# Kernel tuning notes

Hardware: AMD Instinct MI355X
Metric: run time of the kernel (lower is better)

Reference implementation:

```python
import jax, jax.numpy as jnp
import numpy as np

B, S, D, H, FF = 4, 2048, 1024, 16, 4096
DT, TARGET, ITERS = 0.1, 0.0, 5


def _ln(x, w, b):
    mu = jnp.mean(x, axis=-1, keepdims=True)
    var = jnp.mean((x - mu) ** 2, axis=-1, keepdims=True)
    return (x - mu) * jax.lax.rsqrt(var + 1e-5) * w + b


def setup_inputs() -> dict:
    key = jax.random.key(0)
    ks = iter(jax.random.split(key, 16))
    w = lambda shape: jax.random.normal(next(ks), shape, dtype=jnp.float32) * 0.02
    return {
        "x": jax.random.normal(next(ks), (B, S, D), dtype=jnp.float32),
        "ln_attn_w": jnp.ones((D,), jnp.float32), "ln_attn_b": jnp.zeros((D,), jnp.float32),
        "attn_in_w": w((3 * D, D)), "attn_in_b": jnp.zeros((3 * D,), jnp.float32),
        "attn_out_w": w((D, D)), "attn_out_b": jnp.zeros((D,), jnp.float32),
        "ln1_w": jnp.ones((D,), jnp.float32), "ln1_b": jnp.zeros((D,), jnp.float32),
        "ln2_w": jnp.ones((D,), jnp.float32), "ln2_b": jnp.zeros((D,), jnp.float32),
        "inl_u_w": w((D, D)), "inl_u_b": jnp.zeros((D,), jnp.float32),
        "inl_a_w": w((D, D)), "inl_a_b": jnp.zeros((D,), jnp.float32),
        "inl_b_w": w((D, D)), "inl_b_b": jnp.zeros((D,), jnp.float32),
        "inl_g_w": w((D, D)), "inl_g_b": jnp.zeros((D,), jnp.float32),
        "ff1_w": w((FF, D)), "ff1_b": jnp.zeros((FF,), jnp.float32),
        "ff2_w": w((D, FF)), "ff2_b": jnp.zeros((D,), jnp.float32),
    }


def reference(x, ln_attn_w, ln_attn_b, attn_in_w, attn_in_b, attn_out_w, attn_out_b,
              ln1_w, ln1_b, ln2_w, ln2_b,
              inl_u_w, inl_u_b, inl_a_w, inl_a_b, inl_b_w, inl_b_b, inl_g_w, inl_g_b,
              ff1_w, ff1_b, ff2_w, ff2_b):
    dh = D // H
    scale = 1.0 / np.sqrt(dh).astype(np.float32)
    # --- causal multi-head attention (dropout = identity, eval mode) ---
    xn = _ln(x, ln_attn_w, ln_attn_b)
    qkv = xn @ attn_in_w.T + attn_in_b            # [B,S,3D]
    q, k, v = jnp.split(qkv, 3, axis=-1)
    hsplit = lambda t: t.reshape(B, S, H, dh).transpose(0, 2, 1, 3)  # [B,H,S,dh]
    q, k, v = hsplit(q), hsplit(k), hsplit(v)
    scores = jnp.einsum('bhqd,bhkd->bhqk', q, k) * scale
    causal = jnp.triu(jnp.ones((S, S), dtype=bool), 1)
    scores = jnp.where(causal, jnp.finfo(scores.dtype).min, scores)
    probs = jax.nn.softmax(scores, axis=-1)
    attn_out = jnp.einsum('bhqk,bhkd->bhqd', probs, v).transpose(0, 2, 1, 3).reshape(B, S, D)
    attn_out = attn_out @ attn_out_w.T + attn_out_b
    x = x + attn_out
    context = attn_out
    # --- INL integrator dynamics (controllers depend only on context) ---
    xs = _ln(x, ln1_w, ln1_b)
    vs = jnp.zeros_like(xs)
    u = context @ inl_u_w.T + inl_u_b
    alpha = jax.nn.sigmoid(context @ inl_a_w.T + inl_a_b)
    beta = jax.nn.softplus(context @ inl_b_w.T + inl_b_b)
    g = jax.nn.sigmoid(context @ inl_g_w.T + inl_g_b)
    for _ in range(ITERS):
        vs = vs + DT * (alpha * (TARGET - xs) - beta * vs + u)
        xs = xs + DT * g * vs
    x = x + xs
    # --- feed-forward (exact GELU as torch default) ---
    h = _ln(x, ln2_w, ln2_b)
    x = x + (jax.nn.gelu(h @ ff1_w.T + ff1_b, approximate=False) @ ff2_w.T + ff2_b)
    return x
```

## Files before the change

kernel.cpp:

```cpp
#include <hip/hip_runtime.h>
#include <cstdint>
#include <cmath>

typedef __attribute__((ext_vector_type(4))) float floatx4;
typedef __attribute__((ext_vector_type(8))) __bf16 bf16x8;
typedef __attribute__((ext_vector_type(4))) unsigned short ushort4v;

#define DEVI static __device__ __forceinline__

DEVI unsigned short f2b(float f) {
    unsigned x = __float_as_uint(f);
    return (unsigned short)((x + 0x7fffu + ((x >> 16) & 1u)) >> 16);
}
DEVI float b2f(unsigned short u) { return __uint_as_float(((unsigned)u) << 16); }

DEVI void load16(void* lds, const void* g) {
    __builtin_amdgcn_global_load_lds(
        (__attribute__((address_space(1))) void*)(const_cast<void*>(g)),
        (__attribute__((address_space(3))) void*)lds, 16, 0, 0);
}

DEVI floatx4 MFMA16(bf16x8 a, bf16x8 b, floatx4 c) {
    return __builtin_amdgcn_mfma_f32_16x16x32_bf16(a, b, c, 0, 0, 0);
}

__global__ __launch_bounds__(256) void cvt_kernel(const float* __restrict__ src,
                                                  unsigned short* __restrict__ dst, int n4) {
    int i = blockIdx.x * 256 + threadIdx.x;
    if (i >= n4) return;
    floatx4 v = ((const floatx4*)src)[i];
    ushort4v o;
    o[0] = f2b(v[0]); o[1] = f2b(v[1]); o[2] = f2b(v[2]); o[3] = f2b(v[3]);
    ((ushort4v*)dst)[i] = o;
}

__global__ __launch_bounds__(256) void catbias_kernel(const float* __restrict__ a,
                                                      const float* __restrict__ b,
                                                      const float* __restrict__ c,
                                                      const float* __restrict__ d,
                                                      float* __restrict__ o) {
    int i = blockIdx.x * 256 + threadIdx.x;
    int p = i >> 10, j = i & 1023;
    float v = (p == 0) ? a[j] : (p == 1) ? b[j] : (p == 2) ? c[j] : d[j];
    o[i] = v;
}

__global__ __launch_bounds__(256) void ln_kernel(const float* __restrict__ in,
                                                 const float* __restrict__ w,
                                                 const float* __restrict__ b,
                                                 unsigned short* __restrict__ obf,
                                                 float* __restrict__ of) {
    const int row = blockIdx.x, tid = threadIdx.x;
    const floatx4* pr = (const floatx4*)(in + (size_t)row * 1024);
    floatx4 v = pr[tid];
    float s  = v[0] + v[1] + v[2] + v[3];
    float ss = v[0]*v[0] + v[1]*v[1] + v[2]*v[2] + v[3]*v[3];
    #pragma unroll
    for (int o = 32; o >= 1; o >>= 1) { s += __shfl_xor(s, o); ss += __shfl_xor(ss, o); }
    __shared__ float red[8];
    int wv = tid >> 6, lane = tid & 63;
    if (lane == 0) { red[wv] = s; red[4 + wv] = ss; }
    __syncthreads();
    s  = red[0] + red[1] + red[2] + red[3];
    ss = red[4] + red[5] + red[6] + red[7];
    float mu  = s * (1.0f / 1024.0f);
    float var = ss * (1.0f / 1024.0f) - mu * mu;
    float rstd = rsqrtf(var + 1e-5f);
    floatx4 wv4 = ((const floatx4*)w)[tid];
    floatx4 bv4 = ((const floatx4*)b)[tid];
    floatx4 o;
    #pragma unroll
    for (int c = 0; c < 4; c++) o[c] = (v[c] - mu) * rstd * wv4[c] + bv4[c];
    if (obf) {
        ushort4v t;
        t[0] = f2b(o[0]); t[1] = f2b(o[1]); t[2] = f2b(o[2]); t[3] = f2b(o[3]);
        ((ushort4v*)(obf + (size_t)row * 1024))[tid] = t;
    }
    if (of) ((floatx4*)(of + (size_t)row * 1024))[tid] = o;
}

__global__ __launch_bounds__(256) void integrator_kernel(const float* __restrict__ xs0,
                                                         const unsigned short* __restrict__ uabg,
                                                         float* __restrict__ xio) {
    size_t i = (size_t)blockIdx.x * 256 + threadIdx.x;
    size_t tok = i >> 8;
    int grp = (int)(i & 255) * 4;
    const unsigned short* ubase = uabg + tok * 4096 + grp;
    ushort4v uu = *(const ushort4v*)(ubase);
    ushort4v aa = *(const ushort4v*)(ubase + 1024);
    ushort4v bb = *(const ushort4v*)(ubase + 2048);
    ushort4v gg = *(const ushort4v*)(ubase + 3072);
    floatx4 xsv = ((const floatx4*)xs0)[i];
    floatx4 x1  = ((const floatx4*)xio)[i];
    floatx4 res;
    #pragma unroll
    for (int c = 0; c < 4; c++) {
        float u = b2f(uu[c]), a = b2f(aa[c]), bt = b2f(bb[c]), g = b2f(gg[c]);
        float xs = xsv[c], vs = 0.f;
        #pragma unroll
        for (int t = 0; t < 5; t++) {
            vs += 0.1f * (-a * xs - bt * vs + u);
            xs += 0.1f * g * vs;
        }
        res[c] = x1[c] + xs;
    }
    ((floatx4*)xio)[i] = res;
}

template <int EPI, int KP>
__global__ __launch_bounds__(512, 2) void gemm8(const unsigned short* __restrict__ A,
                                                const unsigned short* __restrict__ W,
                                                const float* __restrict__ bias,
                                                unsigned short* __restrict__ ob0,
                                                unsigned short* __restrict__ ob1,
                                                unsigned short* __restrict__ ob2,
                                                float* __restrict__ of0,
                                                const float* __restrict__ xres) {
    constexpr int NT = KP / 64;
    __shared__ unsigned short sA[2][2][256 * 32];
    __shared__ unsigned short sB[2][2][256 * 32];
    const int tid = threadIdx.x;
    const int wave = tid >> 6, lane = tid & 63;
    const int ln = lane & 15, quad = lane >> 4;
    const int wr = wave >> 2, wc = wave & 3;

    const int gx = gridDim.x;
    const int flat = blockIdx.y * gx + blockIdx.x;
    const int cpx = (gx * (int)gridDim.y) >> 3;
    const int rmp = (flat & 7) * cpx + (flat >> 3);
    const size_t m0 = (size_t)(rmp / gx) * 256;
    const int n0 = (rmp % gx) * 256;

    floatx4 acc[8][4];
    #pragma unroll
    for (int mt = 0; mt < 8; mt++)
        #pragma unroll
        for (int nt = 0; nt < 4; nt++) acc[mt][nt] = floatx4{0.f, 0.f, 0.f, 0.f};

    const int srow = tid >> 2;
    const int sgr  = (tid & 3) ^ (srow & 3);
    const unsigned short* gAs = A + (m0 + srow) * KP + sgr * 8;
    const unsigned short* gBs = W + ((size_t)(n0 + srow)) * KP + sgr * 8;
    const size_t jstride = (size_t)128 * KP;
    const int sbase = wave * 512;

    const int csw  = (quad ^ (ln & 3)) * 8;
    const int arow = (wr * 128 + ln) * 32 + csw;
    const int brow = (wc * 64 + ln) * 32 + csw;

    auto stageA = [&](int buf, int kk, int t) {
        const unsigned short* s = gAs + (size_t)t * 64 + kk * 32;
        load16(&sA[buf][kk][sbase], s);
        load16(&sA[buf][kk][sbase + 4096], s + jstride);
    };
    auto stageB = [&](int buf, int kk, int t) {
        const unsigned short* s = gBs + (size_t)t * 64 + kk * 32;
        load16(&sB[buf][kk][sbase], s);
        load16(&sB[buf][kk][sbase + 4096], s + jstride);
    };

    bf16x8 af[8], bq0, bq1;
    auto ldA = [&](int buf, int kk) {
        #pragma unroll
        for (int mt = 0; mt < 8; mt++)
            af[mt] = *(const bf16x8*)&sA[buf][kk][arow + mt * 512];
    };
    auto ldB = [&](int buf, int kk, int nh) {
        bq0 = *(const bf16x8*)&sB[buf][kk][brow + nh * 1024];
        bq1 = *(const bf16x8*)&sB[buf][kk][brow + nh * 1024 + 512];
    };
    auto mma = [&](int nh) {
        __builtin_amdgcn_sched_barrier(0);
        __builtin_amdgcn_s_setprio(1);
        #pragma unroll
        for (int mt = 0; mt < 8; mt++) {
            acc[mt][nh * 2]     = MFMA16(af[mt], bq0, acc[mt][nh * 2]);
            acc[mt][nh * 2 + 1] = MFMA16(af[mt], bq1, acc[mt][nh * 2 + 1]);
        }
        __builtin_amdgcn_s_setprio(0);
        __builtin_amdgcn_sched_barrier(0);
    };

    stageA(0, 0, 0); stageB(0, 0, 0); stageA(0, 1, 0); stageB(0, 1, 0);
    asm volatile("s_waitcnt vmcnt(4)" ::: "memory");
    asm volatile("s_barrier" ::: "memory");

    auto tilestep = [&](int kt, int buf, bool last) {
        ldA(buf, 0); ldB(buf, 0, 0);
        if (!last) stageA(buf ^ 1, 0, kt + 1);
        asm volatile("s_barrier" ::: "memory");
        asm volatile("s_waitcnt lgkmcnt(0)" ::: "memory");
        mma(0);
        asm volatile("s_barrier" ::: "memory");
        ldB(buf, 0, 1);
        if (!last) {
            stageB(buf ^ 1, 0, kt + 1);
            asm volatile("s_waitcnt vmcnt(4)" ::: "memory");
        } else {
            asm volatile("s_waitcnt vmcnt(0)" ::: "memory");
        }
        asm volatile("s_barrier" ::: "memory");
        asm volatile("s_waitcnt lgkmcnt(0)" ::: "memory");
        mma(1);
        asm volatile("s_barrier" ::: "memory");
        ldA(buf, 1); ldB(buf, 1, 0);
        if (!last) stageA(buf ^ 1, 1, kt + 1);
        asm volatile("s_barrier" ::: "memory");
        asm volatile("s_waitcnt lgkmcnt(0)" ::: "memory");
        mma(0);
        asm volatile("s_barrier" ::: "memory");
        ldB(buf, 1, 1);
        if (!last) {
            stageB(buf ^ 1, 1, kt + 1);
            asm volatile("s_waitcnt vmcnt(4)" ::: "memory");
        }
        asm volatile("s_barrier" ::: "memory");
        asm volatile("s_waitcnt lgkmcnt(0)" ::: "memory");
        mma(1);
        asm volatile("s_barrier" ::: "memory");
    };

    #pragma unroll 1
    for (int kt = 0; kt < NT - 2; kt += 2) {
        tilestep(kt, 0, false);
        tilestep(kt + 1, 1, false);
    }
    tilestep(NT - 2, 0, false);
    tilestep(NT - 1, 1, true);

    const size_t rowb = m0 + wr * 128 + quad * 4;
    const int colb = n0 + wc * 64 + ln;
    #pragma unroll
    for (int mt = 0; mt < 8; mt++) {
        #pragma unroll
        for (int nt = 0; nt < 4; nt++) {
            const int n = colb + nt * 16;
            const float bs = bias[n];
            #pragma unroll
            for (int r = 0; r < 4; r++) {
                const size_t row = rowb + mt * 16 + r;
                float c = acc[mt][nt][r] + bs;
                if constexpr (EPI == 0) {
                    int sect = n >> 10, d1 = n & 1023, h = d1 >> 6, d = d1 & 63;
                    int bb = (int)(row >> 11), s = (int)(row & 2047);
                    size_t bh = (size_t)(bb * 16 + h);
                    if (sect == 0)      ob0[(bh * 2048 + s) * 64 + d] = f2b(c);
                    else if (sect == 1) ob1[(bh * 2048 + s) * 64 + d] = f2b(c);
                    else                ob2[(bh * 64 + d) * 2048 + s] = f2b(c);
                } else if constexpr (EPI == 2) {
                    int p = n >> 10;
                    float v;
                    if (p == 0)       v = c;
                    else if (p == 2)  v = fmaxf(c, 0.f) + log1pf(__expf(-fabsf(c)));
                    else              v = 1.f / (1.f + __expf(-c));
                    ob0[row * 4096 + n] = f2b(v);
                } else if constexpr (EPI == 3) {
                    float v = 0.5f * c * (1.f + erff(c * 0.70710678118654752f));
                    ob0[row * 4096 + n] = f2b(v);
                }
            }
        }
    }
}

template <int EPI>
__global__ __launch_bounds__(256, 3) void gemm_bt(const unsigned short* __restrict__ A,
                                                  const unsigned short* __restrict__ W,
                                                  const float* __restrict__ bias, int K,
                                                  unsigned short* __restrict__ ob0,
                                                  unsigned short* __restrict__ ob1,
                                                  unsigned short* __restrict__ ob2,
                                                  float* __restrict__ of0,
                                                  const float* __restrict__ xres) {
    __shared__ unsigned short sA[3][128 * 32];
    __shared__ unsigned short sB[3][128 * 32];
    const int tid = threadIdx.x;
    const int wave = tid >> 6, lane = tid & 63;
    const int ln = lane & 15, quad = lane >> 4;
    const int gx = gridDim.x;
    const int flat = blockIdx.y * gx + blockIdx.x;
    const int cpx = (gx * (int)gridDim.y) >> 3;
    const int rmp = (flat & 7) * cpx + (flat >> 3);
    const size_t m0 = (size_t)(rmp / gx) * 128;
    const int n0 = (rmp % gx) * 128;
    const int wm = (wave >> 1) * 64, wn = (wave & 1) * 64;

    const floatx4 z4 = {0.f, 0.f, 0.f, 0.f};
    floatx4 acc[4][4];
    #pragma unroll
    for (int mt = 0; mt < 4; mt++)
        #pragma unroll
        for (int nt = 0; nt < 4; nt++) acc[mt][nt] = z4;

    const int r16 = lane >> 2;
    const int gsw = (((lane & 3) ^ (r16 & 3) ^ ((r16 >> 2) & 3))) * 8;
    const int arow = wave * 16 + r16;
    const unsigned short* gA = A + (m0 + (size_t)arow) * K + gsw;
    const unsigned short* gB = W + ((size_t)(n0 + arow)) * K + gsw;
    const size_t rs64 = (size_t)64 * K;
    const int so = wave * 512;
    const int swr = ((quad ^ (ln & 3) ^ ((ln >> 2) & 3))) * 8;

    const int T = K >> 5;

    load16(&sA[0][so], gA);
    load16(&sA[0][so + 2048], gA + rs64);
    load16(&sB[0][so], gB);
    load16(&sB[0][so + 2048], gB + rs64);
    load16(&sA[1][so], gA + 32);
    load16(&sA[1][so + 2048], gA + rs64 + 32);
    load16(&sB[1][so], gB + 32);
    load16(&sB[1][so + 2048], gB + rs64 + 32);
    asm volatile("s_waitcnt vmcnt(4)" ::: "memory");
    asm volatile("s_barrier" ::: "memory");

    bf16x8 fa0[4], fb0[4], fa1[4], fb1[4];
    #pragma unroll
    for (int mt = 0; mt < 4; mt++)
        fa0[mt] = *(const bf16x8*)&sA[0][(wm + mt * 16 + ln) * 32 + swr];
    #pragma unroll
    for (int nt = 0; nt < 4; nt++)
        fb0[nt] = *(const bf16x8*)&sB[0][(wn + nt * 16 + ln) * 32 + swr];

    auto step = [&](int t, bf16x8* afc, bf16x8* bfc, bf16x8* afn, bf16x8* bfn) {
        if (t + 2 < T) {
            const int k = (t + 2) * 32;
            const int nb = (t + 2) % 3;
            load16(&sA[nb][so], gA + k);
            load16(&sA[nb][so + 2048], gA + rs64 + k);
            load16(&sB[nb][so], gB + k);
            load16(&sB[nb][so + 2048], gB + rs64 + k);
        }
        __builtin_amdgcn_sched_barrier(0);
        __builtin_amdgcn_s_setprio(1);
        #pragma unroll
        for (int mt = 0; mt < 4; mt++)
            #pragma unroll
            for (int nt = 0; nt < 4; nt++)
                acc[mt][nt] = MFMA16(afc[mt], bfc[nt], acc[mt][nt]);
        __builtin_amdgcn_s_setprio(0);
        __builtin_amdgcn_sched_barrier(0);
        if (t + 1 < T) {
            if (t + 2 < T) {
                asm volatile("s_waitcnt vmcnt(4) lgkmcnt(0)" ::: "memory");
            } else {
                asm volatile("s_waitcnt vmcnt(0) lgkmcnt(0)" ::: "memory");
            }
            asm volatile("s_barrier" ::: "memory");
            const int nb = (t + 1) % 3;
            afn[0] = *(const bf16x8*)&sA[nb][(wm + ln) * 32 + swr];
            #pragma unroll
            for (int nt = 0; nt < 4; nt++)
                bfn[nt] = *(const bf16x8*)&sB[nb][(wn + nt * 16 + ln) * 32 + swr];
            #pragma unroll
            for (int mt = 1; mt < 4; mt++)
                afn[mt] = *(const bf16x8*)&sA[nb][(wm + mt * 16 + ln) * 32 + swr];
        }
    };

    #pragma unroll 1
    for (int t = 0; t < T; t += 2) {
        step(t, fa0, fb0, fa1, fb1);
        step(t + 1, fa1, fb1, fa0, fb0);
    }

    const size_t rowb = m0 + wm + quad * 4;
    const int colb = n0 + wn + ln;
    #pragma unroll
    for (int mt = 0; mt < 4; mt++) {
        #pragma unroll
        for (int nt = 0; nt < 4; nt++) {
            const int n = colb + nt * 16;
            const float bs = bias[n];
            #pragma unroll
            for (int r = 0; r < 4; r++) {
                const size_t row = rowb + mt * 16 + r;
                float c = acc[mt][nt][r] + bs;
                if constexpr (EPI == 1) {
                    size_t idx = row * 1024 + n;
                    ob0[idx] = f2b(c);
                    of0[idx] = xres[idx] + c;
                } else {
                    size_t idx = row * 1024 + n;
                    of0[idx] += c;
                }
            }
        }
    }
}

#define PSTR 72
__global__ __launch_bounds__(256, 3) void attn_kernel(const unsigned short* __restrict__ Qb,
                                                      const unsigned short* __restrict__ Kb,
                                                      const unsigned short* __restrict__ Vtb,
                                                      unsigned short* __restrict__ Ob) {
    __shared__ unsigned short sK[2][64 * 64];
    __shared__ unsigned short sVt[2][64 * 64];
    __shared__ unsigned short sQP[128 * PSTR];
    const int pr = blockIdx.x;
    const int bh = blockIdx.y;
    const int tid = threadIdx.x, wave = tid >> 6, lane = tid & 63;
    const int ln = lane & 15, quad = lane >> 4;
    const unsigned short* Q  = Qb  + (size_t)bh * 2048 * 64;
    const unsigned short* Kp = Kb  + (size_t)bh * 2048 * 64;
    const unsigned short* Vt = Vtb + (size_t)bh * 64 * 2048;

    const int rl  = lane >> 3;
    const int gsw = (((lane & 7) ^ rl)) * 8;
    const int sseg = wave * 2;
    const unsigned short* kbase = Kp + (size_t)(sseg * 8 + rl) * 64 + gsw;
    const unsigned short* vbase = Vt + (size_t)(sseg * 8 + rl) * 2048 + gsw;
    unsigned short* sP = &sQP[wave * 32 * PSTR];
    const int bb = bh >> 4, h = bh & 15;
    const floatx4 z4 = {0.f, 0.f, 0.f, 0.f};

    #pragma unroll 1
    for (int phase = 0; phase < 2; phase++) {
        const int qt = phase ? pr : (15 - pr);
        const int q0 = qt * 128;
        const int T = 2 * qt + 2;

        #pragma unroll
        for (int i = 0; i < 4; i++) {
            int s = wave * 4 + i;
            load16(&sQP[s * 512], Q + (size_t)(q0 + s * 8 + rl) * 64 + gsw);
        }
        load16(&sK[0][sseg * 512], kbase);
        load16(&sK[0][(sseg + 1) * 512], kbase + (size_t)8 * 64);
        load16(&sVt[0][sseg * 512], vbase);
        load16(&sVt[0][(sseg + 1) * 512], vbase + (size_t)8 * 2048);
        asm volatile("s_waitcnt vmcnt(0)" ::: "memory");
        asm volatile("s_barrier" ::: "memory");

        bf16x8 aq[2][2];
        #pragma unroll
        for (int mt = 0; mt < 2; mt++)
            #pragma unroll
            for (int ks = 0; ks < 2; ks++)
                aq[mt][ks] = *(const bf16x8*)&sQP[(wave * 32 + mt * 16 + ln) * 64 +
                                                  (((ks * 4 + quad) ^ (ln & 7)) * 8)];
        asm volatile("s_waitcnt lgkmcnt(0)" ::: "memory");
        asm volatile("s_barrier" ::: "memory");

        floatx4 Oacc[2][4];
        float m_run[2][4], l_run[2][4];
        #pragma unroll
        for (int mt = 0; mt < 2; mt++)
            #pragma unroll
            for (int j = 0; j < 4; j++) { Oacc[mt][j] = z4; m_run[mt][j] = -1e30f; l_run[mt][j] = 0.f; }

        const int wave_first = q0 + wave * 32;
        const int wave_last  = wave_first + 31;

        #pragma unroll 1
        for (int t = 0; t < T; t++) {
            const int kk0 = t * 64;
            const int cur = t & 1;
            if (t + 1 < T) {
                const unsigned short* kg = kbase + (size_t)(kk0 + 64) * 64;
                const unsigned short* vg = vbase + (size_t)(kk0 + 64);
                load16(&sK[cur ^ 1][sseg * 512], kg);
                load16(&sK[cur ^ 1][(sseg + 1) * 512], kg + (size_t)8 * 64);
                load16(&sVt[cur ^ 1][sseg * 512], vg);
                load16(&sVt[cur ^ 1][(sseg + 1) * 512], vg + (size_t)8 * 2048);
                asm volatile("s_waitcnt vmcnt(4)" ::: "memory");
            } else {
                asm volatile("s_waitcnt vmcnt(0)" ::: "memory");
            }
            asm volatile("s_barrier" ::: "memory");

            if (kk0 <= wave_last) {
                floatx4 Sc[2][4];
                #pragma unroll
                for (int mt = 0; mt < 2; mt++)
                    #pragma unroll
                    for (int nt = 0; nt < 4; nt++) Sc[mt][nt] = z4;
                __builtin_amdgcn_s_setprio(1);
                #pragma unroll
                for (int ks = 0; ks < 2; ks++) {
                    #pragma unroll
                    for (int nt = 0; nt < 4; nt++) {
                        bf16x8 bk = *(const bf16x8*)&sK[cur][(nt * 16 + ln) * 64 +
                                                             (((ks * 4 + quad) ^ (ln & 7)) * 8)];
                        #pragma unroll
                        for (int mt = 0; mt < 2; mt++)
                            Sc[mt][nt] = MFMA16(aq[mt][ks], bk, Sc[mt][nt]);
                    }
                }
                __builtin_amdgcn_s_setprio(0);
                const bool diag = (kk0 + 63 > wave_first);
                #pragma unroll
                for (int mt = 0; mt < 2; mt++)
                    #pragma unroll
                    for (int nt = 0; nt < 4; nt++)
                        #pragma unroll
                        for (int r = 0; r < 4; r++) {
                            float v = Sc[mt][nt][r] * 0.125f;
                            if (diag) {
                                int rowg = wave_first + mt * 16 + quad * 4 + r;
                                int colg = kk0 + nt * 16 + ln;
                                if (colg > rowg) v = -1e30f;
                            }
                            Sc[mt][nt][r] = v;
                        }
                float alpha[2][4];
                #pragma unroll
                for (int mt = 0; mt < 2; mt++)
                    #pragma unroll
                    for (int r = 0; r < 4; r++) {
                        float mx = fmaxf(fmaxf(Sc[mt][0][r], Sc[mt][1][r]), fmaxf(Sc[mt][2][r], Sc[mt][3][r]));
                        #pragma unroll
                        for (int off = 1; off < 16; off <<= 1) mx = fmaxf(mx, __shfl_xor(mx, off));
                        float mnew = fmaxf(m_run[mt][r], mx);
                        alpha[mt][r] = __expf(m_run[mt][r] - mnew);
                        m_run[mt][r] = mnew;
                    }
                #pragma unroll
                for (int mt = 0; mt < 2; mt++)
                    #pragma unroll
                    for (int r = 0; r < 4; r++) {
                        float rs = 0.f;
                        #pragma unroll
                        for (int nt = 0; nt < 4; nt++) {
                            float p = __expf(Sc[mt][nt][r] - m_run[mt][r]);
                            Sc[mt][nt][r] = p;
                            rs += p;
                        }
                        #pragma unroll
                        for (int off = 1; off < 16; off <<= 1) rs += __shfl_xor(rs, off);
                        l_run[mt][r] = l_run[mt][r] * alpha[mt][r] + rs;
                    }
                #pragma unroll
                for (int mt = 0; mt < 2; mt++)
                    #pragma unroll
                    for (int nt = 0; nt < 4; nt++)
                        #pragma unroll
                        for (int r = 0; r < 4; r++) Oacc[mt][nt][r] *= alpha[mt][r];
                #pragma unroll
                for (int mt = 0; mt < 2; mt++)
                    #pragma unroll
                    for (int nt = 0; nt < 4; nt++)
                        #pragma unroll
                        for (int r = 0; r < 4; r++)
                            sP[(mt * 16 + quad * 4 + r) * PSTR + nt * 16 + ln] = f2b(Sc[mt][nt][r]);
                __builtin_amdgcn_s_setprio(1);
                #pragma unroll
                for (int kp = 0; kp < 2; kp++) {
                    bf16x8 ap[2];
                    #pragma unroll
                    for (int mt = 0; mt < 2; mt++)
                        ap[mt] = *(const bf16x8*)&sP[(mt * 16 + ln) * PSTR + kp * 32 + quad * 8];
                    #pragma unroll
                    for (int nt = 0; nt < 4; nt++) {
                        bf16x8 bv = *(const bf16x8*)&sVt[cur][(nt * 16 + ln) * 64 +
                                                              (((kp * 4 + quad) ^ (ln & 7)) * 8)];
                        #pragma unroll
                        for (int mt = 0; mt < 2; mt++)
                            Oacc[mt][nt] = MFMA16(ap[mt], bv, Oacc[mt][nt]);
                    }
                }
                __builtin_amdgcn_s_setprio(0);
            }
            asm volatile("s_barrier" ::: "memory");
        }

        #pragma unroll
        for (int mt = 0; mt < 2; mt++)
            #pragma unroll
            for (int nt = 0; nt < 4; nt++)
                #pragma unroll
                for (int r = 0; r < 4; r++) {
                    float o = Oacc[mt][nt][r] / l_run[mt][r];
                    int srow = q0 + wave * 32 + mt * 16 + quad * 4 + r;
                    size_t tok = (size_t)bb * 2048 + srow;
                    Ob[tok * 1024 + h * 64 + nt * 16 + ln] = f2b(o);
                }
    }
}

extern "C" void kernel_launch(void* const* d_in, const int* in_sizes, int n_in,
                              void* d_out, int out_size, void* d_ws, size_t ws_size,
                              hipStream_t stream) {
    const float* x          = (const float*)d_in[0];
    const float* ln_attn_w  = (const float*)d_in[1];
    const float* ln_attn_b  = (const float*)d_in[2];
    const float* attn_in_w  = (const float*)d_in[3];
    const float* attn_in_b  = (const float*)d_in[4];
    const float* attn_out_w = (const float*)d_in[5];
    const float* attn_out_b = (const float*)d_in[6];
    const float* ln1_w      = (const float*)d_in[7];
    const float* ln1_b      = (const float*)d_in[8];
    const float* ln2_w      = (const float*)d_in[9];
    const float* ln2_b      = (const float*)d_in[10];
    const float* inl_u_w    = (const float*)d_in[11];
    const float* inl_u_b    = (const float*)d_in[12];
    const float* inl_a_w    = (const float*)d_in[13];
    const float* inl_a_b    = (const float*)d_in[14];
    const float* inl_b_w    = (const float*)d_in[15];
    const float* inl_b_b    = (const float*)d_in[16];
    const float* inl_g_w    = (const float*)d_in[17];
    const float* inl_g_b    = (const float*)d_in[18];
    const float* ff1_w      = (const float*)d_in[19];
    const float* ff1_b      = (const float*)d_in[20];
    const float* ff2_w      = (const float*)d_in[21];
    const float* ff2_b      = (const float*)d_in[22];
    float* out = (float*)d_out;

    char* ws = (char*)d_ws;
    unsigned short* Wqkv  = (unsigned short*)(ws);
    unsigned short* Wout  = (unsigned short*)(ws + 6291456);
    unsigned short* Winl  = (unsigned short*)(ws + 8388608);
    unsigned short* Wff1  = (unsigned short*)(ws + 16777216);
    unsigned short* Wff2  = (unsigned short*)(ws + 25165824);
    unsigned short* xnb   = (unsigned short*)(ws + 33554432);
    unsigned short* qb    = (unsigned short*)(ws + 50331648);
    unsigned short* kb    = (unsigned short*)(ws + 67108864);
    unsigned short* vtb   = (unsigned short*)(ws + 83886080);
    unsigned short* attnb = (unsigned short*)(ws + 100663296);
    unsigned short* ctxb  = (unsigned short*)(ws + 117440512);
    float*          xs    = (float*)(ws + 134217728);
    float*          bias4 = (float*)(ws + 167772160);
    unsigned short* uabg  = (unsigned short*)(ws + 50331648);
    unsigned short* ff1b  = (unsigned short*)(ws + 50331648);

    cvt_kernel<<<3072, 256, 0, stream>>>(attn_in_w, Wqkv, 786432);
    cvt_kernel<<<1024, 256, 0, stream>>>(attn_out_w, Wout, 262144);
    cvt_kernel<<<1024, 256, 0, stream>>>(inl_u_w, Winl + 0, 262144);
    cvt_kernel<<<1024, 256, 0, stream>>>(inl_a_w, Winl + 1048576, 262144);
    cvt_kernel<<<1024, 256, 0, stream>>>(inl_b_w, Winl + 2097152, 262144);
    cvt_kernel<<<1024, 256, 0, stream>>>(inl_g_w, Winl + 3145728, 262144);
    cvt_kernel<<<4096, 256, 0, stream>>>(ff1_w, Wff1, 1048576);
    cvt_kernel<<<4096, 256, 0, stream>>>(ff2_w, Wff2, 1048576);
    catbias_kernel<<<16, 256, 0, stream>>>(inl_u_b, inl_a_b, inl_b_b, inl_g_b, bias4);

    ln_kernel<<<8192, 256, 0, stream>>>(x, ln_attn_w, ln_attn_b, xnb, nullptr);
    gemm8<0, 1024><<<dim3(12, 32), 512, 0, stream>>>(xnb, Wqkv, attn_in_b, qb, kb, vtb, nullptr, nullptr);
    attn_kernel<<<dim3(8, 64), 256, 0, stream>>>(qb, kb, vtb, attnb);
    gemm_bt<1><<<dim3(8, 64), 256, 0, stream>>>(attnb, Wout, attn_out_b, 1024, ctxb, nullptr, nullptr, out, x);
    ln_kernel<<<8192, 256, 0, stream>>>(out, ln1_w, ln1_b, nullptr, xs);
    gemm8<2, 1024><<<dim3(16, 32), 512, 0, stream>>>(ctxb, Winl, bias4, uabg, nullptr, nullptr, nullptr, nullptr);
    integrator_kernel<<<8192, 256, 0, stream>>>(xs, uabg, out);
    ln_kernel<<<8192, 256, 0, stream>>>(out, ln2_w, ln2_b, xnb, nullptr);
    gemm8<3, 1024><<<dim3(16, 32), 512, 0, stream>>>(xnb, Wff1, ff1_b, ff1b, nullptr, nullptr, nullptr, nullptr);
    gemm_bt<4><<<dim3(8, 64), 256, 0, stream>>>(ff1b, Wff2, ff2_b, 4096, nullptr, nullptr, nullptr, out, nullptr);
}
```

Before: 912.5 us.

## Replace 8-phase GEMM pipeline with simpler double-buffered full-tile staging

The 256x256 GEMM kernel drops its fine-grained 8-phase schedule, in which A and B half-tiles were staged in interleaved chunks with many barriers. It now prefetches a full 64-wide K tile of A and B into the other buffer, then runs two 32-wide MFMA sweeps over all 8x4 output tiles. The aim is to cut barrier and waitcnt overhead and give longer uninterrupted MFMA bursts. In exchange, the LDS layout loses its XOR swizzle, which may cause bank conflicts, and only one barrier per K tile limits fine overlap. Unused pointer arguments are also removed from both GEMM kernels.

```diff
diff --git a/kernel.cpp b/kernel.cpp
--- a/kernel.cpp
+++ b/kernel.cpp
@@ -108,17 +108,15 @@
 }
 
 template <int EPI, int KP>
-__global__ __launch_bounds__(512, 2) void gemm8(const unsigned short* __restrict__ A,
-                                                const unsigned short* __restrict__ W,
-                                                const float* __restrict__ bias,
-                                                unsigned short* __restrict__ ob0,
-                                                unsigned short* __restrict__ ob1,
-                                                unsigned short* __restrict__ ob2,
-                                                float* __restrict__ of0,
-                                                const float* __restrict__ xres) {
+__global__ __launch_bounds__(512, 2) void gemm2p(const unsigned short* __restrict__ A,
+                                                 const unsigned short* __restrict__ W,
+                                                 const float* __restrict__ bias,
+                                                 unsigned short* __restrict__ ob0,
+                                                 unsigned short* __restrict__ ob1,
+                                                 unsigned short* __restrict__ ob2) {
     constexpr int NT = KP / 64;
-    __shared__ unsigned short sA[2][2][256 * 32];
-    __shared__ unsigned short sB[2][2][256 * 32];
+    __shared__ unsigned short sA[2][256 * 64];
+    __shared__ unsigned short sB[2][256 * 64];
     const int tid = threadIdx.x;
     const int wave = tid >> 6, lane = tid & 63;
     const int ln = lane & 15, quad = lane >> 4;
@@ -137,96 +135,80 @@
         #pragma unroll
         for (int nt = 0; nt < 4; nt++) acc[mt][nt] = floatx4{0.f, 0.f, 0.f, 0.f};
 
-    const int srow = tid >> 2;
-    const int sgr  = (tid & 3) ^ (srow & 3);
-    const unsigned short* gAs = A + (m0 + srow) * KP + sgr * 8;
-    const unsigned short* gBs = W + ((size_t)(n0 + srow)) * KP + sgr * 8;
-    const size_t jstride = (size_t)128 * KP;
-    const int sbase = wave * 512;
-
-    const int csw  = (quad ^ (ln & 3)) * 8;
-    const int arow = (wr * 128 + ln) * 32 + csw;
-    const int brow = (wc * 64 + ln) * 32 + csw;
-
-    auto stageA = [&](int buf, int kk, int t) {
-        const unsigned short* s = gAs + (size_t)t * 64 + kk * 32;
-        load16(&sA[buf][kk][sbase], s);
-        load16(&sA[buf][kk][sbase + 4096], s + jstride);
+    const int srow = tid >> 3;
+    const unsigned short* gAs = A + (m0 + srow) * KP + (tid & 7) * 8;
+    const unsigned short* gBs = W + ((size_t)(n0 + srow)) * KP + (tid & 7) * 8;
+    const size_t rstride = (size_t)64 * KP;
+    const int lbase = wave * 512;
+
+    auto stage = [&](int buf, int t) {
+        const unsigned short* a = gAs + (size_t)t * 64;
+        const unsigned short* b = gBs + (size_t)t * 64;
+        #pragma unroll
+        for (int j = 0; j < 4; j++)
+            load16(&sA[buf][j * 4096 + lbase], a + j * rstride);
+        #pragma unroll
+        for (int j = 0; j < 4; j++)
+            load16(&sB[buf][j * 4096 + lbase], b + j * rstride);
     };
-    auto stageB = [&](int buf, int kk, int t) {
-        const unsigned short* s = gBs + (size_t)t * 64 + kk * 32;
-        load16(&sB[buf][kk][sbase], s);
-        load16(&sB[buf][kk][sbase + 4096], s + jstride);
+
+    const int abase = (wr * 128 + ln) * 64 + quad * 8;
+    const int bbase = (wc * 64 + ln) * 64 + quad * 8;
+    bf16x8 af[8], bf[4];
+    auto ldA = [&](int buf, int kk) {
+        #pragma unroll
+        for (int mt = 0; mt < 8; mt++)
+            af[mt] = *(const bf16x8*)&sA[buf][abase + mt * 1024 + kk * 32];
     };
-
-    bf16x8 af[8], bq0, bq1;
-    auto ldA = [&](int buf, int kk) {
+    auto ldB = [&](int buf, int kk) {
+        #pragma unroll
+        for (int nt = 0; nt < 4; nt++)
+            bf[nt] = *(const bf16x8*)&sB[buf][bbase + nt * 1024 + kk * 32];
+    };
+    auto mmah = [&]() {
         #pragma unroll
         for (int mt = 0; mt < 8; mt++)
-            af[mt] = *(const bf16x8*)&sA[buf][kk][arow + mt * 512];
+            #pragma unroll
+            for (int nt = 0; nt < 4; nt++)
+                acc[mt][nt] = MFMA16(af[mt], bf[nt], acc[mt][nt]);
     };
-    auto ldB = [&](int buf, int kk, int nh) {
-        bq0 = *(const bf16x8*)&sB[buf][kk][brow + nh * 1024];
-        bq1 = *(const bf16x8*)&sB[buf][kk][brow + nh * 1024 + 512];
-    };
-    auto mma = [&](int nh) {
+
+    stage(0, 0);
+    asm volatile("s_waitcnt vmcnt(0)" ::: "memory");
+    asm volatile("s_barrier" ::: "memory");
+
+    #pragma unroll 1
+    for (int t = 0; t < NT - 1; t++) {
+        const int c = t & 1;
+        stage(c ^ 1, t + 1);
+        __builtin_amdgcn_sched_barrier(0);
+        ldA(c, 0); ldB(c, 0);
+        asm volatile("s_waitcnt lgkmcnt(0)" ::: "memory");
         __builtin_amdgcn_sched_barrier(0);
         __builtin_amdgcn_s_setprio(1);
-        #pragma unroll
-        for (int mt = 0; mt < 8; mt++) {
-            acc[mt][nh * 2]     = MFMA16(af[mt], bq0, acc[mt][nh * 2]);
-            acc[mt][nh * 2 + 1] = MFMA16(af[mt], bq1, acc[mt][nh * 2 + 1]);
-        }
+        mmah();
         __builtin_amdgcn_s_setprio(0);
-        __builtin_amdgcn_sched_barrier(0);
-    };
-
-    stageA(0, 0, 0); stageB(0, 0, 0); stageA(0, 1, 0); stageB(0, 1, 0);
-    asm volatile("s_waitcnt vmcnt(4)" ::: "memory");
-    asm volatile("s_barrier" ::: "memory");
-
-    auto tilestep = [&](int kt, int buf, bool last) {
-        ldA(buf, 0); ldB(buf, 0, 0);
-        if (!last) stageA(buf ^ 1, 0, kt + 1);
+        ldA(c, 1); ldB(c, 1);
+        asm volatile("s_waitcnt lgkmcnt(0)" ::: "memory");
+        __builtin_amdgcn_sched_barrier(0);
+        __builtin_amdgcn_s_setprio(1);
+        mmah();
+        __builtin_amdgcn_s_setprio(0);
+        __builtin_amdgcn_sched_barrier(0);
+        asm volatile("s_waitcnt vmcnt(0)" ::: "memory");
         asm volatile("s_barrier" ::: "memory");
+    }
+    {
+        const int c = (NT - 1) & 1;
+        ldA(c, 0); ldB(c, 0);
         asm volatile("s_waitcnt lgkmcnt(0)" ::: "memory");
-        mma(0);
-        asm volatile("s_barrier" ::: "memory");
-        ldB(buf, 0, 1);
-        if (!last) {
-            stageB(buf ^ 1, 0, kt + 1);
-            asm volatile("s_waitcnt vmcnt(4)" ::: "memory");
-        } else {
-            asm volatile("s_waitcnt vmcnt(0)" ::: "memory");
-        }
-        asm volatile("s_barrier" ::: "memory");
+        __builtin_amdgcn_sched_barrier(0);
+        mmah();
+        ldA(c, 1); ldB(c, 1);
         asm volatile("s_waitcnt lgkmcnt(0)" ::: "memory");
-        mma(1);
-        asm volatile("s_barrier" ::: "memory");
-        ldA(buf, 1); ldB(buf, 1, 0);
-        if (!last) stageA(buf ^ 1, 1, kt + 1);
-        asm volatile("s_barrier" ::: "memory");
-        asm volatile("s_waitcnt lgkmcnt(0)" ::: "memory");
-        mma(0);
-        asm volatile("s_barrier" ::: "memory");
-        ldB(buf, 1, 1);
-        if (!last) {
-            stageB(buf ^ 1, 1, kt + 1);
-            asm volatile("s_waitcnt vmcnt(4)" ::: "memory");
-        }
-        asm volatile("s_barrier" ::: "memory");
-        asm volatile("s_waitcnt lgkmcnt(0)" ::: "memory");
-        mma(1);
-        asm volatile("s_barrier" ::: "memory");
-    };
-
-    #pragma unroll 1
-    for (int kt = 0; kt < NT - 2; kt += 2) {
-        tilestep(kt, 0, false);
-        tilestep(kt + 1, 1, false);
-    }
-    tilestep(NT - 2, 0, false);
-    tilestep(NT - 1, 1, true);
+        __builtin_amdgcn_sched_barrier(0);
+        mmah();
+    }
 
     const size_t rowb = m0 + wr * 128 + quad * 4;
     const int colb = n0 + wc * 64 + ln;
@@ -254,7 +236,7 @@
                     else if (p == 2)  v = fmaxf(c, 0.f) + log1pf(__expf(-fabsf(c)));
                     else              v = 1.f / (1.f + __expf(-c));
                     ob0[row * 4096 + n] = f2b(v);
-                } else if constexpr (EPI == 3) {
+                } else {
                     float v = 0.5f * c * (1.f + erff(c * 0.70710678118654752f));
                     ob0[row * 4096 + n] = f2b(v);
                 }
@@ -268,8 +250,6 @@
                                                   const unsigned short* __restrict__ W,
                                                   const float* __restrict__ bias, int K,
                                                   unsigned short* __restrict__ ob0,
-                                                  unsigned short* __restrict__ ob1,
-                                                  unsigned short* __restrict__ ob2,
                                                   float* __restrict__ of0,
                                                   const float* __restrict__ xres) {
     __shared__ unsigned short sA[3][128 * 32];
@@ -634,13 +614,13 @@
     catbias_kernel<<<16, 256, 0, stream>>>(inl_u_b, inl_a_b, inl_b_b, inl_g_b, bias4);
 
     ln_kernel<<<8192, 256, 0, stream>>>(x, ln_attn_w, ln_attn_b, xnb, nullptr);
-    gemm8<0, 1024><<<dim3(12, 32), 512, 0, stream>>>(xnb, Wqkv, attn_in_b, qb, kb, vtb, nullptr, nullptr);
+    gemm2p<0, 1024><<<dim3(12, 32), 512, 0, stream>>>(xnb, Wqkv, attn_in_b, qb, kb, vtb);
     attn_kernel<<<dim3(8, 64), 256, 0, stream>>>(qb, kb, vtb, attnb);
-    gemm_bt<1><<<dim3(8, 64), 256, 0, stream>>>(attnb, Wout, attn_out_b, 1024, ctxb, nullptr, nullptr, out, x);
+    gemm_bt<1><<<dim3(8, 64), 256, 0, stream>>>(attnb, Wout, attn_out_b, 1024, ctxb, out, x);
     ln_kernel<<<8192, 256, 0, stream>>>(out, ln1_w, ln1_b, nullptr, xs);
-    gemm8<2, 1024><<<dim3(16, 32), 512, 0, stream>>>(ctxb, Winl, bias4, uabg, nullptr, nullptr, nullptr, nullptr);
+    gemm2p<2, 1024><<<dim3(16, 32), 512, 0, stream>>>(ctxb, Winl, bias4, uabg, nullptr, nullptr);
     integrator_kernel<<<8192, 256, 0, stream>>>(xs, uabg, out);
     ln_kernel<<<8192, 256, 0, stream>>>(out, ln2_w, ln2_b, xnb, nullptr);
-    gemm8<3, 1024><<<dim3(16, 32), 512, 0, stream>>>(xnb, Wff1, ff1_b, ff1b, nullptr, nullptr, nullptr, nullptr);
-    gemm_bt<4><<<dim3(8, 64), 256, 0, stream>>>(ff1b, Wff2, ff2_b, 4096, nullptr, nullptr, nullptr, out, nullptr);
-}
+    gemm2p<3, 1024><<<dim3(16, 32), 512, 0, stream>>>(xnb, Wff1, ff1_b, ff1b, nullptr, nullptr);
+    gemm_bt<4><<<dim3(8, 64), 256, 0, stream>>>(ff1b, Wff2, ff2_b, 4096, nullptr, out, nullptr);
+}
```

New measurement: 924.2 us. No clear change (+1.3%).
